# Kernel optimization log

Measured on AMD Instinct MI355X. Metric: run time of the kernel, lower is better.

The kernel has to match this reference:

```python
import jax, jax.numpy as jnp
import numpy as np

B, C, H, Wd = 4096, 32, 14, 14
ENC_DIM = 512
ATT_DIM = 128


def setup_inputs() -> dict:
    key = jax.random.key(0)
    ks = jax.random.split(key, 10)
    s = 0.05
    return {
        "img_features": jax.random.normal(ks[0], (B, C, H, Wd), jnp.float32),
        "prev_hidden": jax.random.normal(ks[1], (B, ENC_DIM), jnp.float32),
        "W_w": jax.random.normal(ks[2], (ATT_DIM, C), jnp.float32) * s,
        "W_b": jnp.zeros((ATT_DIM,), jnp.float32),
        "U_w": jax.random.normal(ks[3], (ATT_DIM, ENC_DIM), jnp.float32) * s,
        "U_b": jnp.zeros((ATT_DIM,), jnp.float32),
        "v_w": jax.random.normal(ks[4], (1, ATT_DIM), jnp.float32) * s,
        "v_b": jnp.zeros((1,), jnp.float32),
        "fb_w": jax.random.normal(ks[5], (C, ENC_DIM), jnp.float32) * s,
        "fb_b": jnp.zeros((C,), jnp.float32),
    }


def reference(img_features, prev_hidden, W_w, W_b, U_w, U_b, v_w, v_b, fb_w, fb_b):
    b = img_features.shape[0]
    c = img_features.shape[1]
    # [B, C, H, W] -> [B, P, C] where P = H*W (spatial positions)
    img_parts = img_features.reshape(b, c, -1).transpose(0, 2, 1)
    W_s = jnp.einsum('bpc,ac->bpa', img_parts, W_w) + W_b          # [B, P, 128]
    U_h = prev_hidden @ U_w.T + U_b                                 # [B, 128]
    att = jnp.tanh(W_s + U_h[:, None, :])                           # [B, P, 128]
    score = jnp.einsum('bpa,a->bp', att, v_w[0]) + v_b[0]           # [B, P]
    att_weights = jax.nn.softmax(score, axis=1)                     # softmax over spatial
    context = jnp.einsum('bpc,bp->bc', img_parts, att_weights)      # [B, 32]
    beta = jax.nn.sigmoid(prev_hidden @ fb_w.T + fb_b)              # [B, 32]
    context = context * beta
    return (context, att_weights)
```

## Files before the change

kernel.cpp:

```cpp
#include <hip/hip_runtime.h>
#include <hip/hip_bf16.h>


typedef __attribute__((ext_vector_type(8))) short short8;
typedef __attribute__((ext_vector_type(8))) __bf16 bf16x8;
typedef __attribute__((ext_vector_type(4))) float floatx4;

static __device__ __forceinline__ float bf2f(unsigned short u) {
    union { unsigned int i; float f; } v; v.i = ((unsigned int)u) << 16; return v.f;
}
static __device__ __forceinline__ unsigned short f2bf(float f) {
    union { float f; unsigned int i; } v; v.f = f;
    unsigned int r = v.i + 0x7FFFu + ((v.i >> 16) & 1u);
    return (unsigned short)(r >> 16);
}
static __device__ __forceinline__ float fast_tanh(float x) {
    return 1.0f - 2.0f / (1.0f + __expf(2.0f * x));
}
static __device__ __forceinline__ void split8(const float* src, bf16x8* hi, bf16x8* lo) {
    short8 h8, l8;
#pragma unroll
    for (int j = 0; j < 8; j++) {
        float x = src[j];
        unsigned short h = f2bf(x);
        h8[j] = (short)h;
        l8[j] = (short)f2bf(x - bf2f(h));
    }
    *hi = __builtin_bit_cast(bf16x8, h8);
    *lo = __builtin_bit_cast(bf16x8, l8);
}

__global__ __launch_bounds__(256) void k0_split(
    const float* __restrict__ U_w, const float* __restrict__ fb_w,
    const float* __restrict__ W_w,
    unsigned short* __restrict__ Bhi, unsigned short* __restrict__ Blo,
    unsigned short* __restrict__ Whi, unsigned short* __restrict__ Wlo)
{
    int i = blockIdx.x * 256 + threadIdx.x;
    float x;
    if (i < 65536) x = U_w[i];
    else if (i < 81920) x = fb_w[i - 65536];
    else x = W_w[i - 81920];
    unsigned short h = f2bf(x);
    unsigned short l = f2bf(x - bf2f(h));
    if (i < 81920) { Bhi[i] = h; Blo[i] = l; }
    else { Whi[i - 81920] = h; Wlo[i - 81920] = l; }
}

__global__ __launch_bounds__(256) void k1_uh_beta(
    const float* __restrict__ hidden,
    const unsigned short* __restrict__ Bhi,
    const unsigned short* __restrict__ Blo,
    const float* __restrict__ U_b, const float* __restrict__ W_b,
    const float* __restrict__ fb_b,
    float* __restrict__ uh_out,
    float* __restrict__ beta_out)
{
    __shared__ float s_part[4 * 2560];
    const int tid = threadIdx.x;
    const int wave = tid >> 6, lane = tid & 63, quad = lane >> 4, l16 = lane & 15;
    const int mtile = blockIdx.x;
    const int arow = mtile * 16 + l16;

    floatx4 acc[10];
#pragma unroll
    for (int i = 0; i < 10; i++) acc[i] = (floatx4)(0.0f);

#pragma unroll
    for (int ksi = 0; ksi < 4; ksi++) {
        const int e0 = (wave * 4 + ksi) * 32 + quad * 8;
        bf16x8 ah, al;
        split8(hidden + (size_t)arow * 512 + e0, &ah, &al);
#pragma unroll
        for (int n = 0; n < 10; n++) {
            const size_t bo = (size_t)(n * 16 + l16) * 512 + e0;
            bf16x8 bh = *(const bf16x8*)(Bhi + bo);
            bf16x8 bl = *(const bf16x8*)(Blo + bo);
            acc[n] = __builtin_amdgcn_mfma_f32_16x16x32_bf16(ah, bl, acc[n], 0, 0, 0);
            acc[n] = __builtin_amdgcn_mfma_f32_16x16x32_bf16(al, bh, acc[n], 0, 0, 0);
            acc[n] = __builtin_amdgcn_mfma_f32_16x16x32_bf16(ah, bh, acc[n], 0, 0, 0);
        }
    }
#pragma unroll
    for (int n = 0; n < 10; n++)
#pragma unroll
        for (int r = 0; r < 4; r++)
            s_part[wave * 2560 + (quad * 4 + r) * 160 + n * 16 + l16] = acc[n][r];
    __syncthreads();

#pragma unroll
    for (int j = 0; j < 10; j++) {
        const int i = tid + j * 256;
        float v = s_part[i] + s_part[2560 + i] + s_part[5120 + i] + s_part[7680 + i];
        const int m = mtile * 16 + i / 160, col = i % 160;
        if (col < 128) {
            uh_out[(size_t)m * 128 + col] = v + U_b[col] + W_b[col];
        } else {
            const int c = col - 128;
            beta_out[(size_t)m * 32 + c] = 1.0f / (1.0f + __expf(-(v + fb_b[c])));
        }
    }
}

#define PSTR 40
#define PROWS 208

__global__ __launch_bounds__(256) void k2_attn(
    const float* __restrict__ img,
    const unsigned short* __restrict__ Whi,
    const unsigned short* __restrict__ Wlo,
    const float* __restrict__ v_w,
    const float* __restrict__ uh,
    const float* __restrict__ beta,
    float* __restrict__ out)
{
    __shared__ __align__(16) unsigned short s_hi[PROWS * PSTR];
    __shared__ __align__(16) unsigned short s_lo[PROWS * PSTR];
    __shared__ float s_uhv[256];
    __shared__ float s_score[200];
    __shared__ float s_red[8];
    __shared__ float s_ctx[4][32];

    const int tid = threadIdx.x;
    const int b = blockIdx.x;
    const int wave = tid >> 6, lane = tid & 63, quad = lane >> 4, l16 = lane & 15;

    if (tid < 196) {
        float v[32];
#pragma unroll
        for (int c = 0; c < 32; c++)
            v[c] = img[(size_t)b * 6272 + c * 196 + tid];
        const int base = tid * PSTR;
#pragma unroll
        for (int g = 0; g < 4; g++) {
            short8 h8, l8;
#pragma unroll
            for (int j = 0; j < 8; j++) {
                float x = v[g * 8 + j];
                unsigned short h = f2bf(x);
                h8[j] = (short)h;
                l8[j] = (short)f2bf(x - bf2f(h));
            }
            *(short8*)&s_hi[base + g * 8] = h8;
            *(short8*)&s_lo[base + g * 8] = l8;
        }
    } else {
        for (int i = tid - 196; i < 480; i += 60) {
            s_hi[196 * PSTR + i] = 0;
            s_lo[196 * PSTR + i] = 0;
        }
    }
    if (tid < 128) s_uhv[tid] = uh[(size_t)b * 128 + tid];
    else s_uhv[tid] = v_w[tid - 128];

    bf16x8 bh[8], bl[8];
#pragma unroll
    for (int nt = 0; nt < 8; nt++) {
        const int a = nt * 16 + l16;
        bh[nt] = *(const bf16x8*)(Whi + a * 32 + quad * 8);
        bl[nt] = *(const bf16x8*)(Wlo + a * 32 + quad * 8);
    }
    __syncthreads();

    for (int mt = wave; mt < 13; mt += 4) {
        const int p_lane = mt * 16 + l16;
        bf16x8 ah = *(const bf16x8*)&s_hi[p_lane * PSTR + quad * 8];
        bf16x8 al = *(const bf16x8*)&s_lo[p_lane * PSTR + quad * 8];
        float sc[4] = {0.f, 0.f, 0.f, 0.f};
#pragma unroll
        for (int nt = 0; nt < 8; nt++) {
            floatx4 d = (floatx4)(0.0f);
            d = __builtin_amdgcn_mfma_f32_16x16x32_bf16(ah, bl[nt], d, 0, 0, 0);
            d = __builtin_amdgcn_mfma_f32_16x16x32_bf16(al, bh[nt], d, 0, 0, 0);
            d = __builtin_amdgcn_mfma_f32_16x16x32_bf16(ah, bh[nt], d, 0, 0, 0);
            const int a = nt * 16 + l16;
            const float va = s_uhv[128 + a], ua = s_uhv[a];
#pragma unroll
            for (int r = 0; r < 4; r++)
                sc[r] += va * fast_tanh(d[r] + ua);
        }
#pragma unroll
        for (int r = 0; r < 4; r++) {
            sc[r] += __shfl_xor(sc[r], 1);
            sc[r] += __shfl_xor(sc[r], 2);
            sc[r] += __shfl_xor(sc[r], 4);
            sc[r] += __shfl_xor(sc[r], 8);
        }
        if (l16 == 0) {
#pragma unroll
            for (int r = 0; r < 4; r++) {
                const int p = mt * 16 + quad * 4 + r;
                if (p < 196) s_score[p] = sc[r];
            }
        }
    }
    __syncthreads();

    float x = (tid < 196) ? s_score[tid] : -1e30f;
    float m = x;
#pragma unroll
    for (int off = 32; off > 0; off >>= 1) m = fmaxf(m, __shfl_xor(m, off));
    if (lane == 0) s_red[wave] = m;
    __syncthreads();
    m = fmaxf(fmaxf(s_red[0], s_red[1]), fmaxf(s_red[2], s_red[3]));
    float e = (tid < 196) ? __expf(x - m) : 0.0f;
    float ssum = e;
#pragma unroll
    for (int off = 32; off > 0; off >>= 1) ssum += __shfl_xor(ssum, off);
    if (lane == 0) s_red[4 + wave] = ssum;
    __syncthreads();
    const float tot = s_red[4] + s_red[5] + s_red[6] + s_red[7];
    const float wgt = e / tot;
    if (tid < 196) {
        s_score[tid] = wgt;
        out[131072 + (size_t)b * 196 + tid] = wgt;
    }
    __syncthreads();

    {
        const int c = lane & 31;
        const int po = wave * 2 + (lane >> 5);
        float acc = 0.0f;
        for (int j = 0; j < 25; j++) {
            const int p = po + j * 8;
            if (p < 196) {
                const int idx = p * PSTR + c;
                acc += (bf2f(s_hi[idx]) + bf2f(s_lo[idx])) * s_score[p];
            }
        }
        acc += __shfl_xor(acc, 32);
        if ((lane >> 5) == 0) s_ctx[wave][c] = acc;
    }
    __syncthreads();
    if (tid < 32) {
        const float v = s_ctx[0][tid] + s_ctx[1][tid] + s_ctx[2][tid] + s_ctx[3][tid];
        out[(size_t)b * 32 + tid] = v * beta[(size_t)b * 32 + tid];
    }
}

extern "C" void kernel_launch(void* const* d_in, const int* in_sizes, int n_in,
                              void* d_out, int out_size, void* d_ws, size_t ws_size,
                              hipStream_t stream) {
    const float* img    = (const float*)d_in[0];
    const float* hidden = (const float*)d_in[1];
    const float* W_w    = (const float*)d_in[2];
    const float* W_b    = (const float*)d_in[3];
    const float* U_w    = (const float*)d_in[4];
    const float* U_b    = (const float*)d_in[5];
    const float* v_w    = (const float*)d_in[6];
    const float* fb_w   = (const float*)d_in[8];
    const float* fb_b   = (const float*)d_in[9];
    float* out = (float*)d_out;

    float* uh_ws   = (float*)d_ws;
    float* beta_ws = uh_ws + 4096 * 128;
    unsigned short* Bhi = (unsigned short*)(beta_ws + 4096 * 32);
    unsigned short* Blo = Bhi + 81920;
    unsigned short* Whi = Blo + 81920;
    unsigned short* Wlo = Whi + 4096;

    k0_split<<<dim3(336), dim3(256), 0, stream>>>(U_w, fb_w, W_w, Bhi, Blo, Whi, Wlo);
    k1_uh_beta<<<dim3(256), dim3(256), 0, stream>>>(hidden, Bhi, Blo, U_b, W_b, fb_b,
                                                    uh_ws, beta_ws);
    k2_attn<<<dim3(4096), dim3(256), 0, stream>>>(img, Whi, Wlo, v_w, uh_ws, beta_ws, out);
}
```

Measured before the change: 239.7 us.

## Split-K hidden GEMM, store fp32 image in LDS, use rcp-based activations

The hidden-state GEMM gains a split-K path, chosen from the available workspace size, that writes partial sums and adds a separate reduction kernel, so more blocks run concurrently. The attention kernel now keeps the image tile in LDS as fp32 and splits it into bf16 hi/lo on the fly by truncation with perm instructions, instead of rounding and storing two bf16 copies. It also hoists the uh and v values into registers, sets launch bounds to target 4 blocks per SM, and replaces divisions with rcp in tanh, sigmoid and the softmax normalisation. The costs are an extra kernel launch plus a pass over the partial buffer, and slightly different rounding.

```diff
diff --git a/kernel.cpp b/kernel.cpp
--- a/kernel.cpp
+++ b/kernel.cpp
@@ -5,6 +5,7 @@
 typedef __attribute__((ext_vector_type(8))) short short8;
 typedef __attribute__((ext_vector_type(8))) __bf16 bf16x8;
 typedef __attribute__((ext_vector_type(4))) float floatx4;
+typedef __attribute__((ext_vector_type(4))) unsigned int uint4v;
 
 static __device__ __forceinline__ float bf2f(unsigned short u) {
     union { unsigned int i; float f; } v; v.i = ((unsigned int)u) << 16; return v.f;
@@ -14,20 +15,34 @@
     unsigned int r = v.i + 0x7FFFu + ((v.i >> 16) & 1u);
     return (unsigned short)(r >> 16);
 }
-static __device__ __forceinline__ float fast_tanh(float x) {
-    return 1.0f - 2.0f / (1.0f + __expf(2.0f * x));
-}
-static __device__ __forceinline__ void split8(const float* src, bf16x8* hi, bf16x8* lo) {
-    short8 h8, l8;
-#pragma unroll
-    for (int j = 0; j < 8; j++) {
-        float x = src[j];
-        unsigned short h = f2bf(x);
-        h8[j] = (short)h;
-        l8[j] = (short)f2bf(x - bf2f(h));
-    }
-    *hi = __builtin_bit_cast(bf16x8, h8);
-    *lo = __builtin_bit_cast(bf16x8, l8);
+static __device__ __forceinline__ float tanh_rcp(float x) {
+    float e = __expf(2.0f * x);
+    float r = __builtin_amdgcn_rcpf(1.0f + e);
+    return __builtin_fmaf(-2.0f, r, 1.0f);
+}
+static __device__ __forceinline__ float sigmoid_rcp(float x) {
+    return __builtin_amdgcn_rcpf(1.0f + __expf(-x));
+}
+static __device__ __forceinline__ void split_trunc8(const float* src, bf16x8* hi, bf16x8* lo) {
+    uint4v u0 = *(const uint4v*)src;
+    uint4v u1 = *(const uint4v*)(src + 4);
+    unsigned int fb[8], lb[8];
+#pragma unroll
+    for (int j = 0; j < 4; j++) { fb[j] = u0[j]; fb[4 + j] = u1[j]; }
+#pragma unroll
+    for (int k = 0; k < 8; k++) {
+        float x = __uint_as_float(fb[k]);
+        float h = __uint_as_float(fb[k] & 0xFFFF0000u);
+        lb[k] = __float_as_uint(x - h);
+    }
+    uint4v hp, lp;
+#pragma unroll
+    for (int j = 0; j < 4; j++) {
+        hp[j] = __builtin_amdgcn_perm(fb[2 * j + 1], fb[2 * j], 0x07060302u);
+        lp[j] = __builtin_amdgcn_perm(lb[2 * j + 1], lb[2 * j], 0x07060302u);
+    }
+    *hi = __builtin_bit_cast(bf16x8, hp);
+    *lo = __builtin_bit_cast(bf16x8, lp);
 }
 
 __global__ __launch_bounds__(256) void k0_split(
@@ -47,30 +62,32 @@
     else { Whi[i - 81920] = h; Wlo[i - 81920] = l; }
 }
 
-__global__ __launch_bounds__(256) void k1_uh_beta(
+__global__ __launch_bounds__(256) void k1_gemm(
     const float* __restrict__ hidden,
     const unsigned short* __restrict__ Bhi,
     const unsigned short* __restrict__ Blo,
     const float* __restrict__ U_b, const float* __restrict__ W_b,
     const float* __restrict__ fb_b,
-    float* __restrict__ uh_out,
-    float* __restrict__ beta_out)
+    float* __restrict__ uh_out, float* __restrict__ beta_out,
+    float* __restrict__ partial, int nsplit, int direct)
 {
     __shared__ float s_part[4 * 2560];
     const int tid = threadIdx.x;
     const int wave = tid >> 6, lane = tid & 63, quad = lane >> 4, l16 = lane & 15;
-    const int mtile = blockIdx.x;
+    const int mtile = blockIdx.x / nsplit;
+    const int kblock = 512 / nsplit;
+    const int ks0 = (blockIdx.x % nsplit) * kblock + wave * (kblock >> 2);
+    const int ksteps = kblock >> 7;
     const int arow = mtile * 16 + l16;
 
     floatx4 acc[10];
 #pragma unroll
     for (int i = 0; i < 10; i++) acc[i] = (floatx4)(0.0f);
 
-#pragma unroll
-    for (int ksi = 0; ksi < 4; ksi++) {
-        const int e0 = (wave * 4 + ksi) * 32 + quad * 8;
+    for (int ksi = 0; ksi < ksteps; ksi++) {
+        const int e0 = ks0 + ksi * 32 + quad * 8;
         bf16x8 ah, al;
-        split8(hidden + (size_t)arow * 512 + e0, &ah, &al);
+        split_trunc8(hidden + (size_t)arow * 512 + e0, &ah, &al);
 #pragma unroll
         for (int n = 0; n < 10; n++) {
             const size_t bo = (size_t)(n * 16 + l16) * 512 + e0;
@@ -92,20 +109,35 @@
     for (int j = 0; j < 10; j++) {
         const int i = tid + j * 256;
         float v = s_part[i] + s_part[2560 + i] + s_part[5120 + i] + s_part[7680 + i];
-        const int m = mtile * 16 + i / 160, col = i % 160;
-        if (col < 128) {
-            uh_out[(size_t)m * 128 + col] = v + U_b[col] + W_b[col];
+        if (direct) {
+            const int m = mtile * 16 + i / 160, col = i % 160;
+            if (col < 128) uh_out[(size_t)m * 128 + col] = v + U_b[col] + W_b[col];
+            else beta_out[(size_t)m * 32 + (col - 128)] = sigmoid_rcp(v + fb_b[col - 128]);
         } else {
-            const int c = col - 128;
-            beta_out[(size_t)m * 32 + c] = 1.0f / (1.0f + __expf(-(v + fb_b[c])));
-        }
-    }
-}
-
-#define PSTR 40
-#define PROWS 208
-
-__global__ __launch_bounds__(256) void k2_attn(
+            partial[(size_t)blockIdx.x * 2560 + i] = v;
+        }
+    }
+}
+
+__global__ __launch_bounds__(256) void k1b_reduce(
+    const float* __restrict__ partial,
+    const float* __restrict__ U_b, const float* __restrict__ W_b,
+    const float* __restrict__ fb_b,
+    float* __restrict__ uh_out, float* __restrict__ beta_out, int nsplit)
+{
+    const int idx = blockIdx.x * 256 + threadIdx.x;
+    const int mt = idx / 2560, r = idx % 2560;
+    float v = 0.0f;
+    for (int s = 0; s < nsplit; s++)
+        v += partial[(size_t)(mt * nsplit + s) * 2560 + r];
+    const int m = mt * 16 + r / 160, col = r % 160;
+    if (col < 128) uh_out[(size_t)m * 128 + col] = v + U_b[col] + W_b[col];
+    else beta_out[(size_t)m * 32 + (col - 128)] = sigmoid_rcp(v + fb_b[col - 128]);
+}
+
+#define FSTR 36
+
+__global__ __launch_bounds__(256, 4) void k2_attn(
     const float* __restrict__ img,
     const unsigned short* __restrict__ Whi,
     const unsigned short* __restrict__ Wlo,
@@ -114,8 +146,7 @@
     const float* __restrict__ beta,
     float* __restrict__ out)
 {
-    __shared__ __align__(16) unsigned short s_hi[PROWS * PSTR];
-    __shared__ __align__(16) unsigned short s_lo[PROWS * PSTR];
+    __shared__ __align__(16) float s_img[208 * FSTR];
     __shared__ float s_uhv[256];
     __shared__ float s_score[200];
     __shared__ float s_red[8];
@@ -126,29 +157,16 @@
     const int wave = tid >> 6, lane = tid & 63, quad = lane >> 4, l16 = lane & 15;
 
     if (tid < 196) {
-        float v[32];
-#pragma unroll
-        for (int c = 0; c < 32; c++)
-            v[c] = img[(size_t)b * 6272 + c * 196 + tid];
-        const int base = tid * PSTR;
-#pragma unroll
-        for (int g = 0; g < 4; g++) {
-            short8 h8, l8;
-#pragma unroll
-            for (int j = 0; j < 8; j++) {
-                float x = v[g * 8 + j];
-                unsigned short h = f2bf(x);
-                h8[j] = (short)h;
-                l8[j] = (short)f2bf(x - bf2f(h));
-            }
-            *(short8*)&s_hi[base + g * 8] = h8;
-            *(short8*)&s_lo[base + g * 8] = l8;
+        const size_t base = (size_t)b * 6272 + tid;
+#pragma unroll
+        for (int g = 0; g < 8; g++) {
+            floatx4 t;
+#pragma unroll
+            for (int j = 0; j < 4; j++) t[j] = img[base + (size_t)(4 * g + j) * 196];
+            *(floatx4*)&s_img[tid * FSTR + 4 * g] = t;
         }
     } else {
-        for (int i = tid - 196; i < 480; i += 60) {
-            s_hi[196 * PSTR + i] = 0;
-            s_lo[196 * PSTR + i] = 0;
-        }
+        for (int i = tid - 196; i < 12 * FSTR; i += 60) s_img[196 * FSTR + i] = 0.0f;
     }
     if (tid < 128) s_uhv[tid] = uh[(size_t)b * 128 + tid];
     else s_uhv[tid] = v_w[tid - 128];
@@ -162,10 +180,17 @@
     }
     __syncthreads();
 
+    float ua[8], va[8];
+#pragma unroll
+    for (int nt = 0; nt < 8; nt++) {
+        ua[nt] = s_uhv[nt * 16 + l16];
+        va[nt] = s_uhv[128 + nt * 16 + l16];
+    }
+
     for (int mt = wave; mt < 13; mt += 4) {
         const int p_lane = mt * 16 + l16;
-        bf16x8 ah = *(const bf16x8*)&s_hi[p_lane * PSTR + quad * 8];
-        bf16x8 al = *(const bf16x8*)&s_lo[p_lane * PSTR + quad * 8];
+        bf16x8 ah, al;
+        split_trunc8(&s_img[p_lane * FSTR + quad * 8], &ah, &al);
         float sc[4] = {0.f, 0.f, 0.f, 0.f};
 #pragma unroll
         for (int nt = 0; nt < 8; nt++) {
@@ -173,11 +198,9 @@
             d = __builtin_amdgcn_mfma_f32_16x16x32_bf16(ah, bl[nt], d, 0, 0, 0);
             d = __builtin_amdgcn_mfma_f32_16x16x32_bf16(al, bh[nt], d, 0, 0, 0);
             d = __builtin_amdgcn_mfma_f32_16x16x32_bf16(ah, bh[nt], d, 0, 0, 0);
-            const int a = nt * 16 + l16;
-            const float va = s_uhv[128 + a], ua = s_uhv[a];
 #pragma unroll
             for (int r = 0; r < 4; r++)
-                sc[r] += va * fast_tanh(d[r] + ua);
+                sc[r] = __builtin_fmaf(va[nt], tanh_rcp(d[r] + ua[nt]), sc[r]);
         }
 #pragma unroll
         for (int r = 0; r < 4; r++) {
@@ -210,7 +233,7 @@
     if (lane == 0) s_red[4 + wave] = ssum;
     __syncthreads();
     const float tot = s_red[4] + s_red[5] + s_red[6] + s_red[7];
-    const float wgt = e / tot;
+    const float wgt = e * __builtin_amdgcn_rcpf(tot);
     if (tid < 196) {
         s_score[tid] = wgt;
         out[131072 + (size_t)b * 196 + tid] = wgt;
@@ -223,10 +246,7 @@
         float acc = 0.0f;
         for (int j = 0; j < 25; j++) {
             const int p = po + j * 8;
-            if (p < 196) {
-                const int idx = p * PSTR + c;
-                acc += (bf2f(s_hi[idx]) + bf2f(s_lo[idx])) * s_score[p];
-            }
+            if (p < 196) acc = __builtin_fmaf(s_img[p * FSTR + c], s_score[p], acc);
         }
         acc += __shfl_xor(acc, 32);
         if ((lane >> 5) == 0) s_ctx[wave][c] = acc;
@@ -258,9 +278,19 @@
     unsigned short* Blo = Bhi + 81920;
     unsigned short* Whi = Blo + 81920;
     unsigned short* Wlo = Whi + 4096;
+    float* partial = (float*)(Wlo + 4096);
+    const size_t fixed_bytes = ((char*)partial) - ((char*)d_ws);
+
+    int nsplit = 1, direct = 1;
+    if (ws_size >= fixed_bytes + (size_t)256 * 4 * 2560 * 4) { nsplit = 4; direct = 0; }
+    else if (ws_size >= fixed_bytes + (size_t)256 * 2 * 2560 * 4) { nsplit = 2; direct = 0; }
+    else if (ws_size >= fixed_bytes + (size_t)256 * 1 * 2560 * 4) { nsplit = 1; direct = 0; }
 
     k0_split<<<dim3(336), dim3(256), 0, stream>>>(U_w, fb_w, W_w, Bhi, Blo, Whi, Wlo);
-    k1_uh_beta<<<dim3(256), dim3(256), 0, stream>>>(hidden, Bhi, Blo, U_b, W_b, fb_b,
-                                                    uh_ws, beta_ws);
+    k1_gemm<<<dim3(256 * nsplit), dim3(256), 0, stream>>>(
+        hidden, Bhi, Blo, U_b, W_b, fb_b, uh_ws, beta_ws, partial, nsplit, direct);
+    if (!direct)
+        k1b_reduce<<<dim3(2560), dim3(256), 0, stream>>>(
+            partial, U_b, W_b, fb_b, uh_ws, beta_ws, nsplit);
     k2_attn<<<dim3(4096), dim3(256), 0, stream>>>(img, Whi, Wlo, v_w, uh_ws, beta_ws, out);
 }
```

New measurement: 211.7 us. -11.7%, faster.
